# Kernel optimization log

Hardware: AMD Instinct MI355X
Metric: run time of the kernel (lower is better)

## Reference

```python
import jax, jax.numpy as jnp
import numpy as np

# dims: batch, seq, d_model, heads, d_ff, experts, top-k, vocab, layers
B, S, D, H, F, E, K, V, L = 2, 1024, 768, 12, 3072, 8, 2, 32000, 2
EPS = 1e-6


def setup_inputs() -> dict:
    key = jax.random.key(0)
    ks = jax.random.split(key, 12)
    n = lambda k, shape: jax.random.normal(k, shape, jnp.float32) * 0.02
    return {
        "tokens": jax.random.randint(ks[0], (B, S), 0, V),
        "emb": n(ks[1], (V, D)),            # token embedding, tied lm_head
        "pos_emb": n(ks[2], (S, D)),        # learned positions (use_rope=False)
        "wq": n(ks[3], (L, D, D)), "bq": jnp.zeros((L, D), jnp.float32),
        "wk": n(ks[4], (L, D, D)), "bk": jnp.zeros((L, D), jnp.float32),
        "wv": n(ks[5], (L, D, D)), "bv": jnp.zeros((L, D), jnp.float32),
        "wo": n(ks[6], (L, D, D)), "bo": jnp.zeros((L, D), jnp.float32),
        "ln1": jnp.ones((L, D), jnp.float32),
        "ln2": jnp.ones((L, D), jnp.float32),
        "gate_w": n(ks[7], (L, D, E)), "gate_b": jnp.zeros((L, E), jnp.float32),
        "w1": n(ks[8], (L, E, D, F)), "b1": jnp.zeros((L, E, F), jnp.float32),
        "w2": n(ks[9], (L, E, F, D)), "b2": jnp.zeros((L, E, D), jnp.float32),
        "ln_f": jnp.ones((D,), jnp.float32),
    }


def rmsnorm(x, w):
    return x * jax.lax.rsqrt(jnp.mean(x * x, axis=-1, keepdims=True) + EPS) * w


def attention(h, wq, bq, wk, bk, wv, bv, wo, bo):
    hd = D // H
    q = (h @ wq + bq).reshape(B, S, H, hd)
    k = (h @ wk + bk).reshape(B, S, H, hd)
    v = (h @ wv + bv).reshape(B, S, H, hd)
    scores = jnp.einsum('bqhd,bkhd->bhqk', q, k) / np.float32(np.sqrt(hd))
    causal = jnp.tril(jnp.ones((S, S), bool))  # mask = tril(ones(S,S))
    scores = jnp.where(causal, scores, jnp.float32(-1e9))
    probs = jax.nn.softmax(scores, axis=-1)
    out = jnp.einsum('bhqk,bkhd->bqhd', probs, v).reshape(B, S, D)
    return out @ wo + bo


def moe(h, gw, gb, w1, b1, w2, b2):
    # router: top-k over gate logits, softmax over the k selected logits
    logits = h @ gw + gb                                   # [B,S,E]
    top_vals, top_idx = jax.lax.top_k(logits, K)           # [B,S,K]
    w = jax.nn.softmax(top_vals, axis=-1)
    # combined per-expert weight = sum over capacity slots of mask*weight
    one_hot = jax.nn.one_hot(top_idx, E, dtype=h.dtype)    # [B,S,K,E]
    cw = jnp.einsum('bsk,bske->bse', w, one_hot)           # [B,S,E]
    # original computes EVERY expert's FFN on the full token batch, masks after
    h1 = jax.nn.gelu(jnp.einsum('bsd,edf->bsef', h, w1) + b1, approximate=False)
    eo = jnp.einsum('bsef,efd->bsed', h1, w2) + b2         # [B,S,E,D]
    return jnp.einsum('bsed,bse->bsd', eo, cw)


def reference(tokens, emb, pos_emb, wq, bq, wk, bk, wv, bv, wo, bo,
              ln1, ln2, gate_w, gate_b, w1, b1, w2, b2, ln_f):
    x = emb[tokens] + pos_emb[None, :S]                    # [B,S,D]
    for l in range(L):
        x = x + attention(rmsnorm(x, ln1[l]), wq[l], bq[l], wk[l], bk[l],
                          wv[l], bv[l], wo[l], bo[l])
        x = x + moe(rmsnorm(x, ln2[l]), gate_w[l], gate_b[l],
                    w1[l], b1[l], w2[l], b2[l])
    x = rmsnorm(x, ln_f)
    return x @ emb.T                                       # tied lm_head -> [B,S,V]
```

## Files before the change

kernel.cpp:

```cpp
#include <hip/hip_runtime.h>
#include <math.h>

#define TT 2048
#define BB 2
#define SS 1024
#define DD 768
#define HH 12
#define FF 3072
#define EE 8
#define VV 32000
#define NLAYER 2
#define QBLK 8

typedef __attribute__((ext_vector_type(8))) short bf16x8;
typedef __attribute__((ext_vector_type(4))) float f32x4;

#define GL16(ldst, gsrc) __builtin_amdgcn_global_load_lds( \
    (const __attribute__((address_space(1))) void*)(gsrc), \
    (__attribute__((address_space(3))) void*)(ldst), 16, 0, 0)

static __device__ __forceinline__ unsigned short f2b(float f) {
  unsigned u = __float_as_uint(f);
  unsigned r = (u + 0x7fffu + ((u >> 16) & 1u)) >> 16;
  return (unsigned short)r;
}
static __device__ __forceinline__ unsigned int pk2(float a, float b) {
  return (unsigned int)f2b(a) | ((unsigned int)f2b(b) << 16);
}

__global__ __launch_bounds__(256) void k_embed(const int* __restrict__ tok,
    const float* __restrict__ emb, const float* __restrict__ pos,
    float* __restrict__ x) {
  int t = blockIdx.x;
  int s = t & (SS - 1);
  int tk = tok[t];
  const float* er = emb + (size_t)tk * DD;
  const float* pr = pos + (size_t)s * DD;
  float* xr = x + (size_t)t * DD;
  for (int d = threadIdx.x; d < DD; d += 256)
    xr[d] = er[d] + pr[d];
}

__global__ __launch_bounds__(256) void k_rmsnorm(const float* __restrict__ x,
    const float* __restrict__ w, float* __restrict__ out,
    unsigned short* __restrict__ outb) {
  int t = blockIdx.x;
  const float* xr = x + (size_t)t * DD;
  int tid = threadIdx.x;
  float v0 = xr[tid], v1 = xr[tid + 256], v2 = xr[tid + 512];
  float ss = v0 * v0 + v1 * v1 + v2 * v2;
  for (int off = 32; off > 0; off >>= 1) ss += __shfl_down(ss, off, 64);
  __shared__ float ps[4];
  int wid = tid >> 6, lane = tid & 63;
  if (lane == 0) ps[wid] = ss;
  __syncthreads();
  float r = rsqrtf((ps[0] + ps[1] + ps[2] + ps[3]) * (1.0f / DD) + 1e-6f);
  float* orow = out + (size_t)t * DD;
  unsigned short* brow = outb + (size_t)t * DD;
  float o0 = v0 * r * w[tid], o1 = v1 * r * w[tid + 256], o2 = v2 * r * w[tid + 512];
  orow[tid] = o0; orow[tid + 256] = o1; orow[tid + 512] = o2;
  brow[tid] = f2b(o0); brow[tid + 256] = f2b(o1); brow[tid + 512] = f2b(o2);
}

__global__ __launch_bounds__(256) void k_tcvt(const float* __restrict__ src,
    unsigned short* __restrict__ dst, int R, int C, size_t srcZ, size_t dstZ) {
  src += (size_t)blockIdx.z * srcZ;
  dst += (size_t)blockIdx.z * dstZ;
  __shared__ unsigned short tile[32][40];
  int t = threadIdx.x;
  int r = t >> 3, c4 = (t & 7) * 4;
  int r0 = blockIdx.y * 32, c0 = blockIdx.x * 32;
  float4 v = *(const float4*)(src + (size_t)(r0 + r) * C + c0 + c4);
  tile[r][c4 + 0] = f2b(v.x); tile[r][c4 + 1] = f2b(v.y);
  tile[r][c4 + 2] = f2b(v.z); tile[r][c4 + 3] = f2b(v.w);
  __syncthreads();
  int cc = t >> 3, r4 = (t & 7) * 4;
  ushort4 o;
  o.x = tile[r4 + 0][cc]; o.y = tile[r4 + 1][cc];
  o.z = tile[r4 + 2][cc]; o.w = tile[r4 + 3][cc];
  *(ushort4*)(dst + (size_t)(c0 + cc) * R + r0 + r4) = o;
}

__global__ __launch_bounds__(256) void k_cvt(const float* __restrict__ src,
    unsigned short* __restrict__ dst) {
  size_t i = ((size_t)blockIdx.x * 256 + threadIdx.x) * 8;
  float4 a = *(const float4*)(src + i);
  float4 b = *(const float4*)(src + i + 4);
  ushort4 o0, o1;
  o0.x = f2b(a.x); o0.y = f2b(a.y); o0.z = f2b(a.z); o0.w = f2b(a.w);
  o1.x = f2b(b.x); o1.y = f2b(b.y); o1.z = f2b(b.z); o1.w = f2b(b.w);
  *(ushort4*)(dst + i) = o0;
  *(ushort4*)(dst + i + 4) = o1;
}

template<bool EXPERT>
__global__ __launch_bounds__(256) void k_skf32(
    const float* __restrict__ A, const float* __restrict__ W0,
    const float* __restrict__ W1, const float* __restrict__ W2,
    float* __restrict__ part, int M, int Ntot, int Nthird, int K, int KC,
    int nsplit, int prows,
    const int* __restrict__ counts, const int* __restrict__ bases) {
  int s, base = 0, cnt = M, sel = 0, n0;
  const float* W;
  if (EXPERT) {
    int z = blockIdx.z;
    s = z % nsplit;
    int e = z / nsplit;
    cnt = counts[e]; base = bases[e];
    W = W0 + (size_t)e * K * Nthird;
    n0 = blockIdx.x * 128;
  } else {
    s = blockIdx.z;
    int tpn = Nthird >> 7;
    sel = blockIdx.x / tpn;
    n0 = (blockIdx.x - sel * tpn) * 128;
    W = sel == 0 ? W0 : sel == 1 ? W1 : W2;
  }
  int m0 = blockIdx.y * 128;
  if (EXPERT && m0 >= cnt) return;
  int kbase = s * KC;

  __shared__ float As[16][132];
  __shared__ float Bs[16][132];
  int tid = threadIdx.x;
  int tx = tid & 15, ty = tid >> 4;
  int ra = tid >> 1, ka0 = (tid & 1) * 8;
  int kb = tid >> 4, nb0 = (tid & 15) * 8;
  bool arow_ok = !EXPERT || (m0 + ra < cnt);
  const float* Arow = A + (size_t)(EXPERT ? (base + m0 + (arow_ok ? ra : 0))
                                          : (m0 + ra)) * K + kbase;
  float acc[8][8] = {};

  float4 av0 = make_float4(0.f, 0.f, 0.f, 0.f), av1 = av0, bv0, bv1;
  if (arow_ok) {
    av0 = *(const float4*)(Arow + ka0);
    av1 = *(const float4*)(Arow + ka0 + 4);
  }
  {
    const float* Wrow = W + (size_t)(kbase + kb) * Nthird + n0 + nb0;
    bv0 = *(const float4*)(Wrow);
    bv1 = *(const float4*)(Wrow + 4);
  }

  for (int k0 = 0; k0 < KC; k0 += 16) {
    As[ka0 + 0][ra] = av0.x; As[ka0 + 1][ra] = av0.y;
    As[ka0 + 2][ra] = av0.z; As[ka0 + 3][ra] = av0.w;
    As[ka0 + 4][ra] = av1.x; As[ka0 + 5][ra] = av1.y;
    As[ka0 + 6][ra] = av1.z; As[ka0 + 7][ra] = av1.w;
    *(float4*)&Bs[kb][nb0] = bv0;
    *(float4*)&Bs[kb][nb0 + 4] = bv1;
    __syncthreads();
    float4 nav0 = make_float4(0.f, 0.f, 0.f, 0.f), nav1 = nav0, nbv0 = nav0, nbv1 = nav0;
    if (k0 + 16 < KC) {
      if (arow_ok) {
        nav0 = *(const float4*)(Arow + k0 + 16 + ka0);
        nav1 = *(const float4*)(Arow + k0 + 16 + ka0 + 4);
      }
      const float* Wn = W + (size_t)(kbase + k0 + 16 + kb) * Nthird + n0 + nb0;
      nbv0 = *(const float4*)(Wn);
      nbv1 = *(const float4*)(Wn + 4);
    }
#pragma unroll
    for (int kk = 0; kk < 16; kk++) {
      float4 a0 = *(const float4*)&As[kk][ty * 8];
      float4 a1 = *(const float4*)&As[kk][ty * 8 + 4];
      float4 b0 = *(const float4*)&Bs[kk][tx * 8];
      float4 b1 = *(const float4*)&Bs[kk][tx * 8 + 4];
      float a[8] = {a0.x, a0.y, a0.z, a0.w, a1.x, a1.y, a1.z, a1.w};
      float b[8] = {b0.x, b0.y, b0.z, b0.w, b1.x, b1.y, b1.z, b1.w};
#pragma unroll
      for (int i = 0; i < 8; i++) {
#pragma unroll
        for (int j = 0; j < 8; j++) acc[i][j] = fmaf(a[i], b[j], acc[i][j]);
      }
    }
    __syncthreads();
    av0 = nav0; av1 = nav1; bv0 = nbv0; bv1 = nbv1;
  }
#pragma unroll
  for (int i = 0; i < 8; i++) {
    int m = m0 + ty * 8 + i;
    if (EXPERT && m >= cnt) continue;
    size_t prow = EXPERT ? ((size_t)s * prows + base + m) : ((size_t)s * M + m);
    float* orow = part + prow * Ntot + sel * Nthird;
#pragma unroll
    for (int j = 0; j < 8; j++)
      orow[n0 + tx * 8 + j] = acc[i][j];
  }
}

__global__ __launch_bounds__(256) void k_qkvred(const float* __restrict__ part,
    const float* __restrict__ bq, const float* __restrict__ bk,
    const float* __restrict__ bv, float* __restrict__ qb,
    float* __restrict__ kb, float* __restrict__ vb) {
  int t = blockIdx.x;
  for (int c = threadIdx.x; c < 2304; c += 256) {
    float v = part[(size_t)t * 2304 + c] + part[((size_t)TT + t) * 2304 + c];
    if (c < 768)       qb[(size_t)t * DD + c] = v + bq[c];
    else if (c < 1536) kb[(size_t)t * DD + c - 768] = v + bk[c - 768];
    else               vb[(size_t)t * DD + c - 1536] = v + bv[c - 1536];
  }
}

__global__ __launch_bounds__(256) void k_ored(const float* __restrict__ part,
    const float* __restrict__ bo, float* __restrict__ x) {
  int t = blockIdx.x;
  for (int d = threadIdx.x; d < DD; d += 256) {
    float v = part[(size_t)t * DD + d]
            + part[((size_t)TT + t) * DD + d]
            + part[((size_t)2 * TT + t) * DD + d]
            + part[((size_t)3 * TT + t) * DD + d];
    x[(size_t)t * DD + d] += v + bo[d];
  }
}

__global__ __launch_bounds__(256) void k_e2red(const float* __restrict__ part,
    const int* __restrict__ rows, const int* __restrict__ tidx,
    const float* __restrict__ tw, const float* __restrict__ b2,
    float* __restrict__ x) {
  int t = blockIdx.x;
  int r0 = rows[t * 2], r1 = rows[t * 2 + 1];
  int e0 = tidx[t * 2], e1 = tidx[t * 2 + 1];
  float w0 = tw[t * 2], w1 = tw[t * 2 + 1];
  for (int d = threadIdx.x; d < DD; d += 256) {
    float v0 = part[(size_t)r0 * DD + d]
             + part[((size_t)4096 + r0) * DD + d]
             + part[((size_t)8192 + r0) * DD + d]
             + part[((size_t)12288 + r0) * DD + d] + b2[e0 * DD + d];
    float v1 = part[(size_t)r1 * DD + d]
             + part[((size_t)4096 + r1) * DD + d]
             + part[((size_t)8192 + r1) * DD + d]
             + part[((size_t)12288 + r1) * DD + d] + b2[e1 * DD + d];
    x[(size_t)t * DD + d] += w0 * v0 + w1 * v1;
  }
}

__global__ __launch_bounds__(256) void k_attn(const float* __restrict__ q,
    const float* __restrict__ k, const float* __restrict__ v, float* __restrict__ ao) {
  int b = blockIdx.z, hh = blockIdx.y, q0 = blockIdx.x * QBLK;
  __shared__ float qs[QBLK][64];
  __shared__ float sc[QBLK][SS];
  __shared__ float red[QBLK][8];
  int tid = threadIdx.x;
  const size_t hoff = (size_t)b * SS * DD + (size_t)hh * 64;
  for (int i = tid; i < QBLK * 64; i += 256) {
    int qi = i >> 6, d = i & 63;
    qs[qi][d] = q[hoff + (size_t)(q0 + qi) * DD + d];
  }
  __syncthreads();
  int kmax = q0 + QBLK;
  for (int j = tid; j < kmax; j += 256) {
    const float* kr = k + hoff + (size_t)j * DD;
    float p[QBLK];
#pragma unroll
    for (int qi = 0; qi < QBLK; qi++) p[qi] = 0.f;
#pragma unroll 4
    for (int c = 0; c < 16; c++) {
      float4 kv = *(const float4*)(kr + c * 4);
#pragma unroll
      for (int qi = 0; qi < QBLK; qi++)
        p[qi] += qs[qi][c * 4] * kv.x + qs[qi][c * 4 + 1] * kv.y +
                 qs[qi][c * 4 + 2] * kv.z + qs[qi][c * 4 + 3] * kv.w;
    }
#pragma unroll
    for (int qi = 0; qi < QBLK; qi++)
      sc[qi][j] = (j <= q0 + qi) ? p[qi] * 0.125f : -1e30f;
  }
  __syncthreads();
  int wid = tid >> 6, lane = tid & 63;
#pragma unroll
  for (int qi = 0; qi < QBLK; qi++) {
    float mx = -1e30f;
    for (int j = tid; j < kmax; j += 256) mx = fmaxf(mx, sc[qi][j]);
    for (int off = 32; off > 0; off >>= 1) mx = fmaxf(mx, __shfl_down(mx, off, 64));
    if (lane == 0) red[qi][wid] = mx;
  }
  __syncthreads();
#pragma unroll
  for (int qi = 0; qi < QBLK; qi++) {
    float mx = fmaxf(fmaxf(red[qi][0], red[qi][1]), fmaxf(red[qi][2], red[qi][3]));
    float s = 0.f;
    for (int j = tid; j < kmax; j += 256) {
      float e = __expf(sc[qi][j] - mx);
      sc[qi][j] = e;
      s += e;
    }
    for (int off = 32; off > 0; off >>= 1) s += __shfl_down(s, off, 64);
    if (lane == 0) red[qi][4 + wid] = s;
  }
  __syncthreads();
  int d = tid & 63, g = tid >> 6;
  {
    int qiA = g, qiB = g + 4;
    float invA = 1.f / (red[qiA][4] + red[qiA][5] + red[qiA][6] + red[qiA][7]);
    float invB = 1.f / (red[qiB][4] + red[qiB][5] + red[qiB][6] + red[qiB][7]);
    int jendA = q0 + qiA + 1;
    int jendB = q0 + qiB + 1;
    const float* vp = v + hoff + d;
    float a0 = 0.f, a1 = 0.f, a2 = 0.f, a3 = 0.f;
    float b0 = 0.f, b1 = 0.f, b2 = 0.f, b3 = 0.f;
    int jA4 = jendA & ~3;
    for (int j = 0; j < jA4; j += 4) {
      float v0 = vp[(size_t)j * DD];
      float v1 = vp[(size_t)(j + 1) * DD];
      float v2 = vp[(size_t)(j + 2) * DD];
      float v3 = vp[(size_t)(j + 3) * DD];
      a0 = fmaf(sc[qiA][j],     v0, a0);
      a1 = fmaf(sc[qiA][j + 1], v1, a1);
      a2 = fmaf(sc[qiA][j + 2], v2, a2);
      a3 = fmaf(sc[qiA][j + 3], v3, a3);
      b0 = fmaf(sc[qiB][j],     v0, b0);
      b1 = fmaf(sc[qiB][j + 1], v1, b1);
      b2 = fmaf(sc[qiB][j + 2], v2, b2);
      b3 = fmaf(sc[qiB][j + 3], v3, b3);
    }
    for (int t = jA4; t < jendA; t++)
      a0 = fmaf(sc[qiA][t], vp[(size_t)t * DD], a0);
    b0 = fmaf(sc[qiB][jA4],     vp[(size_t)jA4 * DD], b0);
    b1 = fmaf(sc[qiB][jA4 + 1], vp[(size_t)(jA4 + 1) * DD], b1);
    b2 = fmaf(sc[qiB][jA4 + 2], vp[(size_t)(jA4 + 2) * DD], b2);
    b3 = fmaf(sc[qiB][jA4 + 3], vp[(size_t)(jA4 + 3) * DD], b3);
    for (int t = jA4 + 4; t < jendB; t++)
      b0 = fmaf(sc[qiB][t], vp[(size_t)t * DD], b0);
    float accA = (a0 + a2) + (a1 + a3);
    float accB = (b0 + b2) + (b1 + b3);
    ao[hoff + (size_t)(q0 + qiA) * DD + d] = accA * invA;
    ao[hoff + (size_t)(q0 + qiB) * DD + d] = accB * invB;
  }
}

__global__ __launch_bounds__(256) void k_gate(const float* __restrict__ h,
    const float* __restrict__ gw, const float* __restrict__ gb,
    float* __restrict__ glog) {
  __shared__ float hr[DD];
  int t = blockIdx.x;
  for (int d = threadIdx.x; d < DD; d += 256) hr[d] = h[(size_t)t * DD + d];
  __syncthreads();
  int e = threadIdx.x >> 5, j = threadIdx.x & 31;
  float s = 0.f;
  for (int d = j; d < DD; d += 32) s += hr[d] * gw[d * EE + e];
  for (int off = 16; off > 0; off >>= 1) s += __shfl_down(s, off, 32);
  if (j == 0) glog[t * EE + e] = s + gb[e];
}

__global__ void k_zero(int* counts, int* cursor) {
  int i = threadIdx.x;
  if (i < EE) { counts[i] = 0; cursor[i] = 0; }
}

__global__ void k_router(const float* __restrict__ glog, int* __restrict__ tidx,
    float* __restrict__ tw, int* __restrict__ counts) {
  int t = blockIdx.x * 256 + threadIdx.x;
  if (t >= TT) return;
  float l[EE];
#pragma unroll
  for (int e = 0; e < EE; e++) l[e] = glog[t * EE + e];
  int i0 = 0; float v0 = l[0];
#pragma unroll
  for (int e = 1; e < EE; e++) if (l[e] > v0) { v0 = l[e]; i0 = e; }
  int i1 = -1; float v1 = -1e30f;
#pragma unroll
  for (int e = 0; e < EE; e++) if (e != i0 && l[e] > v1) { v1 = l[e]; i1 = e; }
  float e1 = __expf(v1 - v0);
  float inv = 1.f / (1.f + e1);
  tw[t * 2] = inv; tw[t * 2 + 1] = e1 * inv;
  tidx[t * 2] = i0; tidx[t * 2 + 1] = i1;
  atomicAdd(&counts[i0], 1);
  atomicAdd(&counts[i1], 1);
}

__global__ void k_scan(const int* __restrict__ counts, int* __restrict__ bases,
                       int* __restrict__ cursor) {
  int b = 0;
  for (int e = 0; e < EE; e++) { bases[e] = b; cursor[e] = b; b += counts[e]; }
}

__global__ void k_assign(const int* __restrict__ tidx, int* __restrict__ cursor,
                         int* __restrict__ rows, int* __restrict__ gtok) {
  int t = blockIdx.x * 256 + threadIdx.x;
  if (t >= TT) return;
#pragma unroll
  for (int kk = 0; kk < 2; kk++) {
    int e = tidx[t * 2 + kk];
    int r = atomicAdd(&cursor[e], 1);
    rows[t * 2 + kk] = r;
    gtok[r] = t;
  }
}

__global__ __launch_bounds__(256) void k_expert1(const float* __restrict__ h,
    const float* __restrict__ w1, const float* __restrict__ b1,
    const int* __restrict__ gtok, const int* __restrict__ counts,
    const int* __restrict__ bases, float* __restrict__ gh1) {
  int e = blockIdx.z;
  int cnt = counts[e];
  int m0 = blockIdx.y * 128;
  if (m0 >= cnt) return;
  int base = bases[e];
  int n0 = blockIdx.x * 128;
  const float* W = w1 + (size_t)e * DD * FF;
  __shared__ float As[16][132];
  __shared__ float Bs[16][132];
  int tid = threadIdx.x;
  int tx = tid & 15, ty = tid >> 4;
  int ra = tid >> 1, ka0 = (tid & 1) * 8;
  int kb = tid >> 4, nb0 = (tid & 15) * 8;
  int tok = (m0 + ra < cnt) ? gtok[base + m0 + ra] : -1;
  const float* Arow = h + (size_t)(tok < 0 ? 0 : tok) * DD;
  float acc[8][8] = {};

  float4 av0 = make_float4(0.f, 0.f, 0.f, 0.f), av1 = av0, bv0, bv1;
  if (tok >= 0) {
    av0 = *(const float4*)(Arow + ka0);
    av1 = *(const float4*)(Arow + ka0 + 4);
  }
  {
    const float* Wrow = W + (size_t)kb * FF + n0 + nb0;
    bv0 = *(const float4*)(Wrow);
    bv1 = *(const float4*)(Wrow + 4);
  }

  for (int k0 = 0; k0 < DD; k0 += 16) {
    As[ka0 + 0][ra] = av0.x; As[ka0 + 1][ra] = av0.y;
    As[ka0 + 2][ra] = av0.z; As[ka0 + 3][ra] = av0.w;
    As[ka0 + 4][ra] = av1.x; As[ka0 + 5][ra] = av1.y;
    As[ka0 + 6][ra] = av1.z; As[ka0 + 7][ra] = av1.w;
    *(float4*)&Bs[kb][nb0] = bv0;
    *(float4*)&Bs[kb][nb0 + 4] = bv1;
    __syncthreads();
    float4 nav0 = make_float4(0.f, 0.f, 0.f, 0.f), nav1 = nav0, nbv0 = nav0, nbv1 = nav0;
    if (k0 + 16 < DD) {
      if (tok >= 0) {
        nav0 = *(const float4*)(Arow + k0 + 16 + ka0);
        nav1 = *(const float4*)(Arow + k0 + 16 + ka0 + 4);
      }
      const float* Wn = W + (size_t)(k0 + 16 + kb) * FF + n0 + nb0;
      nbv0 = *(const float4*)(Wn);
      nbv1 = *(const float4*)(Wn + 4);
    }
#pragma unroll
    for (int kk = 0; kk < 16; kk++) {
      float4 a0 = *(const float4*)&As[kk][ty * 8];
      float4 a1 = *(const float4*)&As[kk][ty * 8 + 4];
      float4 b0 = *(const float4*)&Bs[kk][tx * 8];
      float4 b1 = *(const float4*)&Bs[kk][tx * 8 + 4];
      float a[8] = {a0.x, a0.y, a0.z, a0.w, a1.x, a1.y, a1.z, a1.w};
      float b[8] = {b0.x, b0.y, b0.z, b0.w, b1.x, b1.y, b1.z, b1.w};
#pragma unroll
      for (int i = 0; i < 8; i++) {
#pragma unroll
        for (int j = 0; j < 8; j++) acc[i][j] = fmaf(a[i], b[j], acc[i][j]);
      }
    }
    __syncthreads();
    av0 = nav0; av1 = nav1; bv0 = nbv0; bv1 = nbv1;
  }
#pragma unroll
  for (int i = 0; i < 8; i++) {
    int m = m0 + ty * 8 + i;
    if (m >= cnt) continue;
    float* orow = gh1 + (size_t)(base + m) * FF;
#pragma unroll
    for (int j = 0; j < 8; j++) {
      int n = n0 + tx * 8 + j;
      float vv = acc[i][j] + b1[e * FF + n];
      orow[n] = 0.5f * vv * (1.f + erff(vv * 0.70710678118654752f));
    }
  }
}

template<bool EXPERT, bool GATHER, bool BIAS, int EPI>
__global__ __launch_bounds__(256) void k_mfma2(
    const unsigned short* __restrict__ A, const unsigned short* __restrict__ Bt,
    const float* __restrict__ bias, void* __restrict__ Cv,
    int M, int N, int K,
    const int* __restrict__ gtok, const int* __restrict__ counts,
    const int* __restrict__ bases) {
  int cnt = M, base = 0;
  if (EXPERT) {
    int e = blockIdx.z;
    cnt = counts[e]; base = bases[e];
    if (BIAS) bias += (size_t)e * N;
    Bt += (size_t)e * N * K;
  }
  int m0 = blockIdx.y * 128;
  if (EXPERT && m0 >= cnt) return;
  int n0 = blockIdx.x * 128;

  __shared__ unsigned short As[128 * 32];
  __shared__ unsigned short Bs[128 * 32];

  int tid = threadIdx.x, lane = tid & 63, w = tid >> 6;
  int r0 = w * 16 + (lane >> 2);
  int r1 = 64 + r0;
  int kc = (lane & 3) * 8;

  const unsigned short *pA0, *pA1;
  if (GATHER) {
    int t0 = (m0 + r0 < cnt) ? gtok[base + m0 + r0] : 0;
    int t1 = (m0 + r1 < cnt) ? gtok[base + m0 + r1] : 0;
    pA0 = A + (size_t)t0 * K + kc;
    pA1 = A + (size_t)t1 * K + kc;
  } else if (EXPERT) {
    int q0_ = (m0 + r0 < cnt) ? base + m0 + r0 : base;
    int q1_ = (m0 + r1 < cnt) ? base + m0 + r1 : base;
    pA0 = A + (size_t)q0_ * K + kc;
    pA1 = A + (size_t)q1_ * K + kc;
  } else {
    pA0 = A + (size_t)(m0 + r0) * K + kc;
    pA1 = A + (size_t)(m0 + r1) * K + kc;
  }
  const unsigned short* pB0 = Bt + (size_t)(n0 + r0) * K + kc;
  const unsigned short* pB1 = Bt + (size_t)(n0 + r1) * K + kc;

  unsigned short* dA0 = As + w * 512;
  unsigned short* dA1 = As + 2048 + w * 512;
  unsigned short* dB0 = Bs + w * 512;
  unsigned short* dB1 = Bs + 2048 + w * 512;

  int wr = w >> 1, wc = w & 1;
  int l15 = lane & 15, lg = lane >> 4;
  const unsigned short* Ar = As + ((wr * 64 + l15) * 32 + lg * 8);
  const unsigned short* Br = Bs + ((wc * 64 + l15) * 32 + lg * 8);

  f32x4 acc[4][4];
#pragma unroll
  for (int i = 0; i < 4; i++)
#pragma unroll
    for (int j = 0; j < 4; j++) acc[i][j] = (f32x4){0.f, 0.f, 0.f, 0.f};

  for (int k0 = 0; k0 < K; k0 += 32) {
    GL16(dA0, pA0 + k0);
    GL16(dA1, pA1 + k0);
    GL16(dB0, pB0 + k0);
    GL16(dB1, pB1 + k0);
    __syncthreads();
    bf16x8 af[4], bfr[4];
#pragma unroll
    for (int f = 0; f < 4; f++) {
      af[f]  = *(const bf16x8*)(Ar + f * 512);
      bfr[f] = *(const bf16x8*)(Br + f * 512);
    }
#pragma unroll
    for (int i = 0; i < 4; i++)
#pragma unroll
      for (int j = 0; j < 4; j++)
        acc[i][j] = __builtin_amdgcn_mfma_f32_16x16x32_bf16(af[i], bfr[j], acc[i][j], 0, 0, 0);
    __syncthreads();
  }

#pragma unroll
  for (int j = 0; j < 4; j++) {
    int n = n0 + wc * 64 + j * 16 + l15;
    float bb = BIAS ? bias[n] : 0.f;
#pragma unroll
    for (int i = 0; i < 4; i++) {
      int mb = m0 + wr * 64 + i * 16 + lg * 4;
#pragma unroll
      for (int r = 0; r < 4; r++) {
        int m = mb + r;
        if (EXPERT && m >= cnt) continue;
        size_t off = (size_t)(base + m) * N + n;
        float v = acc[i][j][r] + bb;
        if (EPI == 0) {
          ((float*)Cv)[off] = v;
        } else {
          float g = 0.5f * v * (1.f + erff(v * 0.70710678118654752f));
          ((unsigned short*)Cv)[off] = f2b(g);
        }
      }
    }
  }
}

__global__ __launch_bounds__(256) void k_mfma_bf32(
    const unsigned short* __restrict__ A, const float* __restrict__ Bf,
    float* __restrict__ C, int M, int N, int K, int mtile0) {
  int m0 = (blockIdx.y + mtile0) * 128;
  int n0 = blockIdx.x * 128;
  __shared__ unsigned short As[128 * 40];
  __shared__ unsigned short Bs[128 * 40];
  int tid = threadIdx.x;
  int srow = tid >> 1;
  int scol = (tid & 1) * 16;
  const unsigned short* arow = A + (size_t)(m0 + srow) * K + scol;
  const float* browf = Bf + (size_t)(n0 + srow) * K + scol;
  unsigned short* As_w = As + srow * 40 + scol;
  unsigned short* Bs_w = Bs + srow * 40 + scol;
  int lane = tid & 63, wid = tid >> 6;
  int wr = wid >> 1, wc = wid & 1;
  int l15 = lane & 15, lg = lane >> 4;
  const unsigned short* Ar = As + ((wr * 64 + l15) * 40 + lg * 8);
  const unsigned short* Br = Bs + ((wc * 64 + l15) * 40 + lg * 8);
  f32x4 acc[4][4];
#pragma unroll
  for (int i = 0; i < 4; i++)
#pragma unroll
    for (int j = 0; j < 4; j++) acc[i][j] = (f32x4){0.f, 0.f, 0.f, 0.f};
  for (int k0 = 0; k0 < K; k0 += 32) {
    uint4 av0 = *(const uint4*)(arow + k0);
    uint4 av1 = *(const uint4*)(arow + k0 + 8);
    float4 f0 = *(const float4*)(browf + k0);
    float4 f1 = *(const float4*)(browf + k0 + 4);
    float4 f2 = *(const float4*)(browf + k0 + 8);
    float4 f3 = *(const float4*)(browf + k0 + 12);
    uint4 bv0 = make_uint4(pk2(f0.x, f0.y), pk2(f0.z, f0.w), pk2(f1.x, f1.y), pk2(f1.z, f1.w));
    uint4 bv1 = make_uint4(pk2(f2.x, f2.y), pk2(f2.z, f2.w), pk2(f3.x, f3.y), pk2(f3.z, f3.w));
    *(uint4*)As_w = av0; *(uint4*)(As_w + 8) = av1;
    *(uint4*)Bs_w = bv0; *(uint4*)(Bs_w + 8) = bv1;
    __syncthreads();
    bf16x8 af[4], bfr[4];
#pragma unroll
    for (int f = 0; f < 4; f++) {
      af[f]  = *(const bf16x8*)(Ar + f * 640);
      bfr[f] = *(const bf16x8*)(Br + f * 640);
    }
#pragma unroll
    for (int i = 0; i < 4; i++)
#pragma unroll
      for (int j = 0; j < 4; j++)
        acc[i][j] = __builtin_amdgcn_mfma_f32_16x16x32_bf16(af[i], bfr[j], acc[i][j], 0, 0, 0);
    __syncthreads();
  }
#pragma unroll
  for (int j = 0; j < 4; j++) {
    int n = n0 + wc * 64 + j * 16 + l15;
#pragma unroll
    for (int i = 0; i < 4; i++) {
      int mb = m0 + wr * 64 + i * 16 + lg * 4;
#pragma unroll
      for (int r = 0; r < 4; r++)
        C[(size_t)(mb + r) * N + n] = acc[i][j][r];
    }
  }
}

__global__ __launch_bounds__(256) void k_scatter(const float* __restrict__ go,
    const int* __restrict__ rows, const float* __restrict__ tw, float* __restrict__ x) {
  int t = blockIdx.x;
  int r0 = rows[t * 2], r1 = rows[t * 2 + 1];
  float w0 = tw[t * 2], w1 = tw[t * 2 + 1];
  float* xr = x + (size_t)t * DD;
  const float* g0 = go + (size_t)r0 * DD;
  const float* g1 = go + (size_t)r1 * DD;
  for (int d = threadIdx.x; d < DD; d += 256)
    xr[d] += w0 * g0[d] + w1 * g1[d];
}

extern "C" void kernel_launch(void* const* d_in, const int* in_sizes, int n_in,
                              void* d_out, int out_size, void* d_ws, size_t ws_size,
                              hipStream_t stream) {
  (void)in_sizes; (void)n_in; (void)out_size;
  const int* tok   = (const int*)d_in[0];
  const float* emb = (const float*)d_in[1];
  const float* pos = (const float*)d_in[2];
  const float* wq  = (const float*)d_in[3];
  const float* bq  = (const float*)d_in[4];
  const float* wk  = (const float*)d_in[5];
  const float* bk  = (const float*)d_in[6];
  const float* wv  = (const float*)d_in[7];
  const float* bvv = (const float*)d_in[8];
  const float* wo  = (const float*)d_in[9];
  const float* bo  = (const float*)d_in[10];
  const float* ln1 = (const float*)d_in[11];
  const float* ln2 = (const float*)d_in[12];
  const float* gw  = (const float*)d_in[13];
  const float* gb  = (const float*)d_in[14];
  const float* w1  = (const float*)d_in[15];
  const float* b1  = (const float*)d_in[16];
  const float* w2  = (const float*)d_in[17];
  const float* b2  = (const float*)d_in[18];
  const float* lnf = (const float*)d_in[19];

  float* ob = (float*)d_out;
  float* fp = ob;
  float* qb   = fp; fp += (size_t)TT * DD;
  float* kb   = fp; fp += (size_t)TT * DD;
  float* vb   = fp; fp += (size_t)TT * DD;
  float* ao   = fp; fp += (size_t)TT * DD;
  float* x    = fp; fp += (size_t)TT * DD;
  float* h    = fp; fp += (size_t)TT * DD;
  float* gh1  = fp; fp += (size_t)TT * 2 * FF;
  float* go   = fp; fp += (size_t)TT * 2 * DD;
  float* glog = fp; fp += (size_t)TT * EE;
  float* tw   = fp; fp += (size_t)TT * 2;
  int* tidx   = (int*)fp; fp += TT * 2;
  int* rows   = (int*)fp; fp += TT * 2;
  int* gtok   = (int*)fp; fp += TT * 2;
  int* counts = (int*)fp; fp += 16;
  int* cursor = (int*)fp; fp += 16;
  int* bases  = (int*)fp; fp += 16;
  unsigned short* hb   = (unsigned short*)fp; fp += (size_t)TT * DD / 2;
  unsigned short* gh1b = (unsigned short*)fp; fp += (size_t)TT * 2 * FF / 2;
  unsigned short* w1t  = (unsigned short*)fp; fp += (size_t)EE * DD * FF / 2;
  unsigned short* w2t  = (unsigned short*)fp; fp += (size_t)EE * FF * DD / 2;
  float* part = fp; fp += (size_t)4 * 4096 * DD;

  unsigned short* hf = (unsigned short*)d_ws;
  bool useWs = ws_size >= (size_t)TT * DD * 2 + (size_t)VV * DD * 2;
  unsigned short* embT = useWs ? (unsigned short*)d_ws + (size_t)TT * DD
                               : (unsigned short*)(ob + 53248000ull);

  k_embed<<<TT, 256, 0, stream>>>(tok, emb, pos, x);
  k_tcvt<<<dim3(96, 24, EE), 256, 0, stream>>>(w1 + (size_t)1 * EE * DD * FF, w1t,
      DD, FF, (size_t)DD * FF, (size_t)DD * FF);
  k_tcvt<<<dim3(24, 96, EE), 256, 0, stream>>>(w2 + (size_t)1 * EE * FF * DD, w2t,
      FF, DD, (size_t)FF * DD, (size_t)FF * DD);

  for (int l = 0; l < NLAYER; l++) {
    const float* wq_l = wq + (size_t)l * DD * DD;
    const float* wk_l = wk + (size_t)l * DD * DD;
    const float* wv_l = wv + (size_t)l * DD * DD;
    const float* wo_l = wo + (size_t)l * DD * DD;

    k_rmsnorm<<<TT, 256, 0, stream>>>(x, ln1 + (size_t)l * DD, h, hb);
    k_skf32<false><<<dim3(18, 16, 2), 256, 0, stream>>>(h, wq_l, wk_l, wv_l,
        part, TT, 2304, 768, 768, 384, 2, TT, nullptr, nullptr);
    k_qkvred<<<TT, 256, 0, stream>>>(part, bq + (size_t)l * DD, bk + (size_t)l * DD,
        bvv + (size_t)l * DD, qb, kb, vb);
    k_attn<<<dim3(SS / QBLK, HH, BB), 256, 0, stream>>>(qb, kb, vb, ao);
    k_skf32<false><<<dim3(6, 16, 4), 256, 0, stream>>>(ao, wo_l, wo_l, wo_l,
        part, TT, 768, 768, 768, 192, 4, TT, nullptr, nullptr);
    k_ored<<<TT, 256, 0, stream>>>(part, bo + (size_t)l * DD, x);

    k_rmsnorm<<<TT, 256, 0, stream>>>(x, ln2 + (size_t)l * DD, h, hb);
    k_gate<<<TT, 256, 0, stream>>>(h, gw + (size_t)l * DD * EE, gb + (size_t)l * EE, glog);
    k_zero<<<1, 64, 0, stream>>>(counts, cursor);
    k_router<<<TT / 256, 256, 0, stream>>>(glog, tidx, tw, counts);
    k_scan<<<1, 1, 0, stream>>>(counts, bases, cursor);
    k_assign<<<TT / 256, 256, 0, stream>>>(tidx, cursor, rows, gtok);
    if (l < NLAYER - 1) {
      k_expert1<<<dim3(FF / 128, TT / 128, EE), 256, 0, stream>>>(
          h, w1 + (size_t)l * EE * DD * FF, b1 + (size_t)l * EE * FF,
          gtok, counts, bases, gh1);
      k_skf32<true><<<dim3(6, 16, 32), 256, 0, stream>>>(gh1,
          w2 + (size_t)l * EE * FF * DD, nullptr, nullptr,
          part, TT, 768, 768, FF, 768, 4, 4096, counts, bases);
      k_e2red<<<TT, 256, 0, stream>>>(part, rows, tidx, tw,
          b2 + (size_t)l * EE * DD, x);
    } else {
      k_mfma2<true, true, true, 2><<<dim3(FF / 128, TT / 128, EE), 256, 0, stream>>>(
          hb, w1t, b1 + (size_t)l * EE * FF, gh1b,
          TT, FF, DD, gtok, counts, bases);
      k_mfma2<true, false, true, 0><<<dim3(DD / 128, TT / 128, EE), 256, 0, stream>>>(
          gh1b, w2t, b2 + (size_t)l * EE * DD, go,
          TT, DD, FF, gtok, counts, bases);
      k_scatter<<<TT, 256, 0, stream>>>(go, rows, tw, x);
    }
  }

  k_cvt<<<(VV * DD) / (256 * 8), 256, 0, stream>>>(emb, embT);
  k_rmsnorm<<<TT, 256, 0, stream>>>(x, lnf, h, hf);
  if (useWs) {
    k_mfma2<false, false, false, 0><<<dim3(VV / 128, 16), 256, 0, stream>>>(
        hf, embT, nullptr, (float*)d_out,
        TT, VV, DD, nullptr, nullptr, nullptr);
  } else {
    k_mfma2<false, false, false, 0><<<dim3(VV / 128, 13), 256, 0, stream>>>(
        hf, embT, nullptr, (float*)d_out,
        TT, VV, DD, nullptr, nullptr, nullptr);
    k_mfma_bf32<<<dim3(VV / 128, 3), 256, 0, stream>>>(
        hf, emb, (float*)d_out, TT, VV, DD, 13);
  }
}
```

Measured before the change: 2.078 ms.

## Fuse residual adds with RMSNorm and gate, merge router kernels into one

Residual reduction kernels (attention output, expert reduce, final scatter) now also compute the following RMSNorm, and the post-attention one also computes the gate logits, so separate rmsnorm and gate launches disappear. The four router kernels (zero, router, scan, assign) become one single-block kernel using shared-memory atomics. This cuts launches and re-reads of the residual stream. The trade-off is a single-block router that serializes over 2048 tokens.

```diff
diff --git a/kernel.cpp b/kernel.cpp
--- a/kernel.cpp
+++ b/kernel.cpp
@@ -28,38 +28,143 @@
   return (unsigned int)f2b(a) | ((unsigned int)f2b(b) << 16);
 }
 
-__global__ __launch_bounds__(256) void k_embed(const int* __restrict__ tok,
+static __device__ __forceinline__ float rms_scale(float v0, float v1, float v2,
+                                                  float* ps, int tid) {
+  float ss = v0 * v0 + v1 * v1 + v2 * v2;
+  for (int off = 32; off > 0; off >>= 1) ss += __shfl_down(ss, off, 64);
+  int wid = tid >> 6, lane = tid & 63;
+  if (lane == 0) ps[wid] = ss;
+  __syncthreads();
+  return rsqrtf((ps[0] + ps[1] + ps[2] + ps[3]) * (1.0f / DD) + 1e-6f);
+}
+
+__global__ __launch_bounds__(256) void k_embed_rms(const int* __restrict__ tok,
     const float* __restrict__ emb, const float* __restrict__ pos,
-    float* __restrict__ x) {
+    const float* __restrict__ w, float* __restrict__ x,
+    float* __restrict__ h, unsigned short* __restrict__ hb) {
   int t = blockIdx.x;
   int s = t & (SS - 1);
   int tk = tok[t];
   const float* er = emb + (size_t)tk * DD;
   const float* pr = pos + (size_t)s * DD;
+  int tid = threadIdx.x;
+  float v0 = er[tid] + pr[tid];
+  float v1 = er[tid + 256] + pr[tid + 256];
+  float v2 = er[tid + 512] + pr[tid + 512];
   float* xr = x + (size_t)t * DD;
-  for (int d = threadIdx.x; d < DD; d += 256)
-    xr[d] = er[d] + pr[d];
-}
-
-__global__ __launch_bounds__(256) void k_rmsnorm(const float* __restrict__ x,
-    const float* __restrict__ w, float* __restrict__ out,
-    unsigned short* __restrict__ outb) {
-  int t = blockIdx.x;
-  const float* xr = x + (size_t)t * DD;
-  int tid = threadIdx.x;
-  float v0 = xr[tid], v1 = xr[tid + 256], v2 = xr[tid + 512];
-  float ss = v0 * v0 + v1 * v1 + v2 * v2;
-  for (int off = 32; off > 0; off >>= 1) ss += __shfl_down(ss, off, 64);
+  xr[tid] = v0; xr[tid + 256] = v1; xr[tid + 512] = v2;
   __shared__ float ps[4];
-  int wid = tid >> 6, lane = tid & 63;
-  if (lane == 0) ps[wid] = ss;
-  __syncthreads();
-  float r = rsqrtf((ps[0] + ps[1] + ps[2] + ps[3]) * (1.0f / DD) + 1e-6f);
-  float* orow = out + (size_t)t * DD;
-  unsigned short* brow = outb + (size_t)t * DD;
+  float r = rms_scale(v0, v1, v2, ps, tid);
   float o0 = v0 * r * w[tid], o1 = v1 * r * w[tid + 256], o2 = v2 * r * w[tid + 512];
+  float* orow = h + (size_t)t * DD;
+  unsigned short* brow = hb + (size_t)t * DD;
   orow[tid] = o0; orow[tid + 256] = o1; orow[tid + 512] = o2;
   brow[tid] = f2b(o0); brow[tid + 256] = f2b(o1); brow[tid + 512] = f2b(o2);
+}
+
+__global__ __launch_bounds__(256) void k_ored_rms_gate(const float* __restrict__ part,
+    const float* __restrict__ bo, const float* __restrict__ w,
+    const float* __restrict__ gw, const float* __restrict__ gb,
+    float* __restrict__ x, float* __restrict__ h, unsigned short* __restrict__ hb,
+    float* __restrict__ glog) {
+  int t = blockIdx.x;
+  int tid = threadIdx.x;
+  float* xr = x + (size_t)t * DD;
+  float v[3];
+#pragma unroll
+  for (int i = 0; i < 3; i++) {
+    int d = tid + i * 256;
+    float s = part[(size_t)t * DD + d]
+            + part[((size_t)TT + t) * DD + d]
+            + part[((size_t)2 * TT + t) * DD + d]
+            + part[((size_t)3 * TT + t) * DD + d];
+    float xn = xr[d] + (s + bo[d]);
+    xr[d] = xn;
+    v[i] = xn;
+  }
+  __shared__ float ps[4];
+  __shared__ float hr[DD];
+  float r = rms_scale(v[0], v[1], v[2], ps, tid);
+  float* orow = h + (size_t)t * DD;
+  unsigned short* brow = hb + (size_t)t * DD;
+#pragma unroll
+  for (int i = 0; i < 3; i++) {
+    int d = tid + i * 256;
+    float o = v[i] * r * w[d];
+    orow[d] = o; brow[d] = f2b(o); hr[d] = o;
+  }
+  __syncthreads();
+  int e = tid >> 5, j = tid & 31;
+  float s = 0.f;
+  for (int d = j; d < DD; d += 32) s += hr[d] * gw[d * EE + e];
+  for (int off = 16; off > 0; off >>= 1) s += __shfl_down(s, off, 32);
+  if (j == 0) glog[t * EE + e] = s + gb[e];
+}
+
+__global__ __launch_bounds__(256) void k_e2red_rms(const float* __restrict__ part,
+    const int* __restrict__ rows, const int* __restrict__ tidx,
+    const float* __restrict__ tw, const float* __restrict__ b2,
+    const float* __restrict__ w, float* __restrict__ x,
+    float* __restrict__ h, unsigned short* __restrict__ hb) {
+  int t = blockIdx.x;
+  int r0 = rows[t * 2], r1 = rows[t * 2 + 1];
+  int e0 = tidx[t * 2], e1 = tidx[t * 2 + 1];
+  float w0 = tw[t * 2], w1 = tw[t * 2 + 1];
+  int tid = threadIdx.x;
+  float* xr = x + (size_t)t * DD;
+  float v[3];
+#pragma unroll
+  for (int i = 0; i < 3; i++) {
+    int d = tid + i * 256;
+    float v0 = part[(size_t)r0 * DD + d]
+             + part[((size_t)4096 + r0) * DD + d]
+             + part[((size_t)8192 + r0) * DD + d]
+             + part[((size_t)12288 + r0) * DD + d] + b2[e0 * DD + d];
+    float v1 = part[(size_t)r1 * DD + d]
+             + part[((size_t)4096 + r1) * DD + d]
+             + part[((size_t)8192 + r1) * DD + d]
+             + part[((size_t)12288 + r1) * DD + d] + b2[e1 * DD + d];
+    float xn = xr[d] + (w0 * v0 + w1 * v1);
+    xr[d] = xn;
+    v[i] = xn;
+  }
+  __shared__ float ps[4];
+  float r = rms_scale(v[0], v[1], v[2], ps, tid);
+  float* orow = h + (size_t)t * DD;
+  unsigned short* brow = hb + (size_t)t * DD;
+#pragma unroll
+  for (int i = 0; i < 3; i++) {
+    int d = tid + i * 256;
+    float o = v[i] * r * w[d];
+    orow[d] = o; brow[d] = f2b(o);
+  }
+}
+
+__global__ __launch_bounds__(256) void k_scatter_rms(const float* __restrict__ go,
+    const int* __restrict__ rows, const float* __restrict__ tw,
+    const float* __restrict__ w, const float* __restrict__ x,
+    unsigned short* __restrict__ hf) {
+  int t = blockIdx.x;
+  int r0 = rows[t * 2], r1 = rows[t * 2 + 1];
+  float w0 = tw[t * 2], w1 = tw[t * 2 + 1];
+  int tid = threadIdx.x;
+  const float* xr = x + (size_t)t * DD;
+  const float* g0 = go + (size_t)r0 * DD;
+  const float* g1 = go + (size_t)r1 * DD;
+  float v[3];
+#pragma unroll
+  for (int i = 0; i < 3; i++) {
+    int d = tid + i * 256;
+    v[i] = xr[d] + (w0 * g0[d] + w1 * g1[d]);
+  }
+  __shared__ float ps[4];
+  float r = rms_scale(v[0], v[1], v[2], ps, tid);
+  unsigned short* brow = hf + (size_t)t * DD;
+#pragma unroll
+  for (int i = 0; i < 3; i++) {
+    int d = tid + i * 256;
+    brow[d] = f2b(v[i] * r * w[d]);
+  }
 }
 
 __global__ __launch_bounds__(256) void k_tcvt(const float* __restrict__ src,
@@ -199,39 +304,6 @@
     if (c < 768)       qb[(size_t)t * DD + c] = v + bq[c];
     else if (c < 1536) kb[(size_t)t * DD + c - 768] = v + bk[c - 768];
     else               vb[(size_t)t * DD + c - 1536] = v + bv[c - 1536];
-  }
-}
-
-__global__ __launch_bounds__(256) void k_ored(const float* __restrict__ part,
-    const float* __restrict__ bo, float* __restrict__ x) {
-  int t = blockIdx.x;
-  for (int d = threadIdx.x; d < DD; d += 256) {
-    float v = part[(size_t)t * DD + d]
-            + part[((size_t)TT + t) * DD + d]
-            + part[((size_t)2 * TT + t) * DD + d]
-            + part[((size_t)3 * TT + t) * DD + d];
-    x[(size_t)t * DD + d] += v + bo[d];
-  }
-}
-
-__global__ __launch_bounds__(256) void k_e2red(const float* __restrict__ part,
-    const int* __restrict__ rows, const int* __restrict__ tidx,
-    const float* __restrict__ tw, const float* __restrict__ b2,
-    float* __restrict__ x) {
-  int t = blockIdx.x;
-  int r0 = rows[t * 2], r1 = rows[t * 2 + 1];
-  int e0 = tidx[t * 2], e1 = tidx[t * 2 + 1];
-  float w0 = tw[t * 2], w1 = tw[t * 2 + 1];
-  for (int d = threadIdx.x; d < DD; d += 256) {
-    float v0 = part[(size_t)r0 * DD + d]
-             + part[((size_t)4096 + r0) * DD + d]
-             + part[((size_t)8192 + r0) * DD + d]
-             + part[((size_t)12288 + r0) * DD + d] + b2[e0 * DD + d];
-    float v1 = part[(size_t)r1 * DD + d]
-             + part[((size_t)4096 + r1) * DD + d]
-             + part[((size_t)8192 + r1) * DD + d]
-             + part[((size_t)12288 + r1) * DD + d] + b2[e1 * DD + d];
-    x[(size_t)t * DD + d] += w0 * v0 + w1 * v1;
   }
 }
 
@@ -329,63 +401,47 @@
   }
 }
 
-__global__ __launch_bounds__(256) void k_gate(const float* __restrict__ h,
-    const float* __restrict__ gw, const float* __restrict__ gb,
-    float* __restrict__ glog) {
-  __shared__ float hr[DD];
-  int t = blockIdx.x;
-  for (int d = threadIdx.x; d < DD; d += 256) hr[d] = h[(size_t)t * DD + d];
-  __syncthreads();
-  int e = threadIdx.x >> 5, j = threadIdx.x & 31;
-  float s = 0.f;
-  for (int d = j; d < DD; d += 32) s += hr[d] * gw[d * EE + e];
-  for (int off = 16; off > 0; off >>= 1) s += __shfl_down(s, off, 32);
-  if (j == 0) glog[t * EE + e] = s + gb[e];
-}
-
-__global__ void k_zero(int* counts, int* cursor) {
-  int i = threadIdx.x;
-  if (i < EE) { counts[i] = 0; cursor[i] = 0; }
-}
-
-__global__ void k_router(const float* __restrict__ glog, int* __restrict__ tidx,
-    float* __restrict__ tw, int* __restrict__ counts) {
-  int t = blockIdx.x * 256 + threadIdx.x;
-  if (t >= TT) return;
-  float l[EE];
-#pragma unroll
-  for (int e = 0; e < EE; e++) l[e] = glog[t * EE + e];
-  int i0 = 0; float v0 = l[0];
-#pragma unroll
-  for (int e = 1; e < EE; e++) if (l[e] > v0) { v0 = l[e]; i0 = e; }
-  int i1 = -1; float v1 = -1e30f;
-#pragma unroll
-  for (int e = 0; e < EE; e++) if (e != i0 && l[e] > v1) { v1 = l[e]; i1 = e; }
-  float e1 = __expf(v1 - v0);
-  float inv = 1.f / (1.f + e1);
-  tw[t * 2] = inv; tw[t * 2 + 1] = e1 * inv;
-  tidx[t * 2] = i0; tidx[t * 2 + 1] = i1;
-  atomicAdd(&counts[i0], 1);
-  atomicAdd(&counts[i1], 1);
-}
-
-__global__ void k_scan(const int* __restrict__ counts, int* __restrict__ bases,
-                       int* __restrict__ cursor) {
-  int b = 0;
-  for (int e = 0; e < EE; e++) { bases[e] = b; cursor[e] = b; b += counts[e]; }
-}
-
-__global__ void k_assign(const int* __restrict__ tidx, int* __restrict__ cursor,
-                         int* __restrict__ rows, int* __restrict__ gtok) {
-  int t = blockIdx.x * 256 + threadIdx.x;
-  if (t >= TT) return;
-#pragma unroll
-  for (int kk = 0; kk < 2; kk++) {
-    int e = tidx[t * 2 + kk];
-    int r = atomicAdd(&cursor[e], 1);
-    rows[t * 2 + kk] = r;
-    gtok[r] = t;
-  }
+__global__ __launch_bounds__(1024) void k_route(const float* __restrict__ glog,
+    int* __restrict__ tidx, float* __restrict__ tw, int* __restrict__ rows,
+    int* __restrict__ gtok, int* __restrict__ counts, int* __restrict__ bases) {
+  __shared__ int cnt_s[EE], base_s[EE], cur_s[EE];
+  int tid = threadIdx.x;
+  if (tid < EE) cnt_s[tid] = 0;
+  __syncthreads();
+  for (int t = tid; t < TT; t += 1024) {
+    float l[EE];
+#pragma unroll
+    for (int e = 0; e < EE; e++) l[e] = glog[t * EE + e];
+    int i0 = 0; float v0 = l[0];
+#pragma unroll
+    for (int e = 1; e < EE; e++) if (l[e] > v0) { v0 = l[e]; i0 = e; }
+    int i1 = -1; float v1 = -1e30f;
+#pragma unroll
+    for (int e = 0; e < EE; e++) if (e != i0 && l[e] > v1) { v1 = l[e]; i1 = e; }
+    float e1 = __expf(v1 - v0);
+    float inv = 1.f / (1.f + e1);
+    tw[t * 2] = inv; tw[t * 2 + 1] = e1 * inv;
+    tidx[t * 2] = i0; tidx[t * 2 + 1] = i1;
+    atomicAdd(&cnt_s[i0], 1);
+    atomicAdd(&cnt_s[i1], 1);
+  }
+  __syncthreads();
+  if (tid == 0) {
+    int b = 0;
+    for (int e = 0; e < EE; e++) { base_s[e] = b; cur_s[e] = b; b += cnt_s[e]; }
+  }
+  __syncthreads();
+  for (int t = tid; t < TT; t += 1024) {
+#pragma unroll
+    for (int kk = 0; kk < 2; kk++) {
+      int e = tidx[t * 2 + kk];
+      int r = atomicAdd(&cur_s[e], 1);
+      rows[t * 2 + kk] = r;
+      gtok[r] = t;
+    }
+  }
+  __syncthreads();
+  if (tid < EE) { counts[tid] = cnt_s[tid]; bases[tid] = base_s[tid]; }
 }
 
 __global__ __launch_bounds__(256) void k_expert1(const float* __restrict__ h,
@@ -633,18 +689,6 @@
         C[(size_t)(mb + r) * N + n] = acc[i][j][r];
     }
   }
-}
-
-__global__ __launch_bounds__(256) void k_scatter(const float* __restrict__ go,
-    const int* __restrict__ rows, const float* __restrict__ tw, float* __restrict__ x) {
-  int t = blockIdx.x;
-  int r0 = rows[t * 2], r1 = rows[t * 2 + 1];
-  float w0 = tw[t * 2], w1 = tw[t * 2 + 1];
-  float* xr = x + (size_t)t * DD;
-  const float* g0 = go + (size_t)r0 * DD;
-  const float* g1 = go + (size_t)r1 * DD;
-  for (int d = threadIdx.x; d < DD; d += 256)
-    xr[d] += w0 * g0[d] + w1 * g1[d];
 }
 
 extern "C" void kernel_launch(void* const* d_in, const int* in_sizes, int n_in,
@@ -695,13 +739,14 @@
   unsigned short* w1t  = (unsigned short*)fp; fp += (size_t)EE * DD * FF / 2;
   unsigned short* w2t  = (unsigned short*)fp; fp += (size_t)EE * FF * DD / 2;
   float* part = fp; fp += (size_t)4 * 4096 * DD;
+  (void)cursor;
 
   unsigned short* hf = (unsigned short*)d_ws;
   bool useWs = ws_size >= (size_t)TT * DD * 2 + (size_t)VV * DD * 2;
   unsigned short* embT = useWs ? (unsigned short*)d_ws + (size_t)TT * DD
                                : (unsigned short*)(ob + 53248000ull);
 
-  k_embed<<<TT, 256, 0, stream>>>(tok, emb, pos, x);
+  k_embed_rms<<<TT, 256, 0, stream>>>(tok, emb, pos, ln1, x, h, hb);
   k_tcvt<<<dim3(96, 24, EE), 256, 0, stream>>>(w1 + (size_t)1 * EE * DD * FF, w1t,
       DD, FF, (size_t)DD * FF, (size_t)DD * FF);
   k_tcvt<<<dim3(24, 96, EE), 256, 0, stream>>>(w2 + (size_t)1 * EE * FF * DD, w2t,
@@ -713,7 +758,6 @@
     const float* wv_l = wv + (size_t)l * DD * DD;
     const float* wo_l = wo + (size_t)l * DD * DD;
 
-    k_rmsnorm<<<TT, 256, 0, stream>>>(x, ln1 + (size_t)l * DD, h, hb);
     k_skf32<false><<<dim3(18, 16, 2), 256, 0, stream>>>(h, wq_l, wk_l, wv_l,
         part, TT, 2304, 768, 768, 384, 2, TT, nullptr, nullptr);
     k_qkvred<<<TT, 256, 0, stream>>>(part, bq + (size_t)l * DD, bk + (size_t)l * DD,
@@ -721,14 +765,10 @@
     k_attn<<<dim3(SS / QBLK, HH, BB), 256, 0, stream>>>(qb, kb, vb, ao);
     k_skf32<false><<<dim3(6, 16, 4), 256, 0, stream>>>(ao, wo_l, wo_l, wo_l,
         part, TT, 768, 768, 768, 192, 4, TT, nullptr, nullptr);
-    k_ored<<<TT, 256, 0, stream>>>(part, bo + (size_t)l * DD, x);
-
-    k_rmsnorm<<<TT, 256, 0, stream>>>(x, ln2 + (size_t)l * DD, h, hb);
-    k_gate<<<TT, 256, 0, stream>>>(h, gw + (size_t)l * DD * EE, gb + (size_t)l * EE, glog);
-    k_zero<<<1, 64, 0, stream>>>(counts, cursor);
-    k_router<<<TT / 256, 256, 0, stream>>>(glog, tidx, tw, counts);
-    k_scan<<<1, 1, 0, stream>>>(counts, bases, cursor);
-    k_assign<<<TT / 256, 256, 0, stream>>>(tidx, cursor, rows, gtok);
+    k_ored_rms_gate<<<TT, 256, 0, stream>>>(part, bo + (size_t)l * DD,
+        ln2 + (size_t)l * DD, gw + (size_t)l * DD * EE, gb + (size_t)l * EE,
+        x, h, hb, glog);
+    k_route<<<1, 1024, 0, stream>>>(glog, tidx, tw, rows, gtok, counts, bases);
     if (l < NLAYER - 1) {
       k_expert1<<<dim3(FF / 128, TT / 128, EE), 256, 0, stream>>>(
           h, w1 + (size_t)l * EE * DD * FF, b1 + (size_t)l * EE * FF,
@@ -736,8 +776,8 @@
       k_skf32<true><<<dim3(6, 16, 32), 256, 0, stream>>>(gh1,
           w2 + (size_t)l * EE * FF * DD, nullptr, nullptr,
           part, TT, 768, 768, FF, 768, 4, 4096, counts, bases);
-      k_e2red<<<TT, 256, 0, stream>>>(part, rows, tidx, tw,
-          b2 + (size_t)l * EE * DD, x);
+      k_e2red_rms<<<TT, 256, 0, stream>>>(part, rows, tidx, tw,
+          b2 + (size_t)l * EE * DD, ln1 + (size_t)(l + 1) * DD, x, h, hb);
     } else {
       k_mfma2<true, true, true, 2><<<dim3(FF / 128, TT / 128, EE), 256, 0, stream>>>(
           hb, w1t, b1 + (size_t)l * EE * FF, gh1b,
@@ -745,12 +785,11 @@
       k_mfma2<true, false, true, 0><<<dim3(DD / 128, TT / 128, EE), 256, 0, stream>>>(
           gh1b, w2t, b2 + (size_t)l * EE * DD, go,
           TT, DD, FF, gtok, counts, bases);
-      k_scatter<<<TT, 256, 0, stream>>>(go, rows, tw, x);
+      k_scatter_rms<<<TT, 256, 0, stream>>>(go, rows, tw, lnf, x, hf);
     }
   }
 
   k_cvt<<<(VV * DD) / (256 * 8), 256, 0, stream>>>(emb, embT);
-  k_rmsnorm<<<TT, 256, 0, stream>>>(x, lnf, h, hf);
   if (useWs) {
     k_mfma2<false, false, false, 0><<<dim3(VV / 128, 16), 256, 0, stream>>>(
         hf, embT, nullptr, (float*)d_out,
```

After: 1.988 ms. -4.3%, faster.
